# Performance work log

Measured on AMD Instinct MI355X. Metric: run time of the kernel, lower is better.

The kernel has to match this reference:

```python
import jax, jax.numpy as jnp
import numpy as np
from jax import lax

B, L, F = 32, 2048, 76   # batch, seq_len, feat_dim
H = 128                  # conv hidden channels
D = 128                  # prototype dim (last 1x1 conv)
P = 128                  # number of prototypes
CLASS_SIZE = 2


def setup_inputs() -> dict:
    key = jax.random.key(0)
    ks = jax.random.split(key, 8)
    w = lambda k, shape: jax.random.normal(k, shape, jnp.float32) * 0.05
    return {
        "x": jax.random.normal(ks[0], (B, L, F), jnp.float32),
        "W1": w(ks[1], (H, F, 5)), "b1": jnp.zeros((H,), jnp.float32),
        "W2": w(ks[2], (H, H, 5)), "b2": jnp.zeros((H,), jnp.float32),
        "W3": w(ks[3], (H, H, 5)), "b3": jnp.zeros((H,), jnp.float32),
        "Wo1": w(ks[4], (D, H)), "bo1": jnp.zeros((D,), jnp.float32),
        "Wo2": w(ks[5], (D, D)), "bo2": jnp.zeros((D,), jnp.float32),
        "prototypes": jax.random.uniform(ks[6], (P, D), jnp.float32),
        "protop_classes": jnp.concatenate([jnp.zeros(P // 2, jnp.int32), jnp.ones(P // 2, jnp.int32)]),
    }


def _conv1d_same(h, W, b):
    # h: (B, C, L), W: (O, C, K=5), symmetric padding 2 == torch padding=k//2
    y = lax.conv_general_dilated(h, W, window_strides=(1,), padding=[(2, 2)],
                                 dimension_numbers=("NCW", "OIW", "NCW"))
    return y + b[None, :, None]


def _maxpool2(h):
    return lax.reduce_window(h, -jnp.inf, lax.max, (1, 1, 2), (1, 1, 2), "VALID")


def reference(x, W1, b1, W2, b2, W3, b3, Wo1, bo1, Wo2, bo2, prototypes, protop_classes):
    h = jnp.transpose(x, (0, 2, 1))  # (B, F, L)
    for W, b in ((W1, b1), (W2, b2), (W3, b3)):
        h = _maxpool2(jax.nn.relu(_conv1d_same(h, W, b)))
    # 1x1 convs as channel matmuls
    h = jax.nn.relu(jnp.einsum("bcl,oc->bol", h, Wo1) + bo1[None, :, None])
    h = jax.nn.relu(jnp.einsum("bcl,oc->bol", h, Wo2) + bo2[None, :, None])
    f = jnp.transpose(h, (0, 2, 1))  # (B, Lp=256, D)
    # l2_conv via ||a-b||^2 = ||a||^2 - 2 a.b + ||b||^2 (same math, GEMM form)
    d2 = (jnp.sum(f * f, axis=-1, keepdims=True)
          - 2.0 * jnp.einsum("bld,pd->blp", f, prototypes)
          + jnp.sum(prototypes * prototypes, axis=-1))  # (B, Lp, P)
    dis = jnp.sqrt(jnp.maximum(d2, 1e-12))
    min_dis = jnp.min(dis, axis=1)  # (B, P): min over patches
    # dis2sim, 'log' activation
    sim = jnp.log((min_dis + 1.0) / (min_dis + 1e-4))
    # init_weights: last_layer.weight[i,j] = 1 if protop_classes[j]==i else -0.5
    lw = jnp.where(protop_classes[None, :] == jnp.arange(CLASS_SIZE)[:, None], 1.0, -0.5)
    out = jax.nn.sigmoid(sim @ lw.T)  # (B, CLASS_SIZE)
    return out, min_dis
```

## Files before the change

### kernel.cpp

```cpp
#include <hip/hip_runtime.h>
#include <cmath>


typedef __attribute__((ext_vector_type(8))) short short8;
typedef __attribute__((ext_vector_type(4))) float f32x4;

__device__ __forceinline__ unsigned short f2bf(float v) {
    union { float f; unsigned u; } x; x.f = v;
    unsigned r = x.u + 0x7fffu + ((x.u >> 16) & 1u);
    return (unsigned short)(r >> 16);
}
__device__ __forceinline__ float bf2f(unsigned short b) {
    union { unsigned u; float f; } x; x.u = ((unsigned)b) << 16;
    return x.f;
}

__device__ void pack_conv_w(int t, int total, const float* __restrict__ W, int C,
                            unsigned short* __restrict__ dst)
{
    if (t >= total) return;
    int lane = t & 63, rest = t >> 6;
    int mf = rest & 7; rest >>= 3;
    int kk = rest % 5, cc = rest / 5;
    int m = mf * 16 + (lane & 15);
    int cb = cc * 32 + (lane >> 4) * 8;
    unsigned short v[8];
#pragma unroll
    for (int j = 0; j < 8; ++j) {
        int c = cb + j;
        v[j] = (c < C) ? f2bf(W[((size_t)m * C + c) * 5 + kk]) : (unsigned short)0;
    }
    *(uint4*)&dst[(size_t)t * 8] = *(uint4*)v;
}

__device__ void pack_mat(int t, const float* __restrict__ M, unsigned short* __restrict__ dst)
{
    if (t >= 2048) return;
    int lane = t & 63, mf = (t >> 6) & 7, cc = t >> 9;
    int m = mf * 16 + (lane & 15);
    int c0 = cc * 32 + (lane >> 4) * 8;
    unsigned short v[8];
#pragma unroll
    for (int j = 0; j < 8; ++j) v[j] = f2bf(M[(size_t)m * 128 + c0 + j]);
    *(uint4*)&dst[(size_t)t * 8] = *(uint4*)v;
}

__global__ __launch_bounds__(256)
void prep_weights_kernel(const float* __restrict__ W1, const float* __restrict__ W2,
                         const float* __restrict__ W3, const float* __restrict__ Wo1,
                         const float* __restrict__ Wo2, const float* __restrict__ protos,
                         unsigned short* A1, unsigned short* A2, unsigned short* A3,
                         unsigned short* AW1, unsigned short* AW2, unsigned short* AP,
                         float* pn, unsigned* pm_bits)
{
    int t = blockIdx.x * 256 + threadIdx.x;
    switch (blockIdx.y) {
    case 0: pack_conv_w(t, 7680,  W1, 76,  A1); break;
    case 1: pack_conv_w(t, 10240, W2, 128, A2); break;
    case 2: pack_conv_w(t, 10240, W3, 128, A3); break;
    case 3: pack_mat(t, Wo1, AW1); break;
    case 4: pack_mat(t, Wo2, AW2); break;
    case 5: pack_mat(t, protos, AP); break;
    case 6:
        if (t < 128) {
            float s = 0.f;
            for (int d = 0; d < 128; ++d) {
                float v = bf2f(f2bf(protos[(size_t)t * 128 + d]));
                s = fmaf(v, v, s);
            }
            pn[t] = s;
        }
        break;
    case 7:
        if (t < 4096) pm_bits[t] = 0x7F800000u;
        break;
    }
}

template <int NJ, int NCC, int STRIDE, int ROWMAX>
__device__ __forceinline__ void conv_k(const unsigned short* __restrict__ Af,
                                       const unsigned short* __restrict__ sIn,
                                       int nbase, int mf0, int lane,
                                       f32x4 (&acc)[4][NJ])
{
    const int lc = lane & 15;
    const int lk = (lane >> 4) * 8;
#pragma unroll
    for (int i = 0; i < 4; ++i)
#pragma unroll
        for (int j = 0; j < NJ; ++j) acc[i][j] = (f32x4){0.f, 0.f, 0.f, 0.f};

    for (int cc = 0; cc < NCC; ++cc) {
#pragma unroll
        for (int kk = 0; kk < 5; ++kk) {
            const int step = cc * 5 + kk;
            short8 a[4];
#pragma unroll
            for (int i = 0; i < 4; ++i)
                a[i] = *(const short8*)&Af[(((size_t)step * 8 + mf0 + i) * 64 + lane) * 8];
            short8 bb[NJ];
#pragma unroll
            for (int j = 0; j < NJ; ++j) {
                int row = nbase + j * 16 + lc + kk;
                if (ROWMAX >= 0) row = min(row, ROWMAX);
                bb[j] = *(const short8*)&sIn[row * STRIDE + cc * 32 + lk];
            }
#pragma unroll
            for (int j = 0; j < NJ; ++j)
#pragma unroll
                for (int i = 0; i < 4; ++i)
                    acc[i][j] = __builtin_amdgcn_mfma_f32_16x16x32_bf16(a[i], bb[j], acc[i][j], 0, 0, 0);
        }
    }
}

__device__ __forceinline__ void gemm_head(const unsigned short* __restrict__ Af,
                                          const unsigned short* __restrict__ s_f,
                                          int mf0h, int lane, f32x4 (&acc)[2])
{
    const int lc = lane & 15;
    const int lk = (lane >> 4) * 8;
    acc[0] = (f32x4){0.f, 0.f, 0.f, 0.f};
    acc[1] = (f32x4){0.f, 0.f, 0.f, 0.f};
#pragma unroll
    for (int cc = 0; cc < 4; ++cc) {
        short8 a[2];
#pragma unroll
        for (int i = 0; i < 2; ++i)
            a[i] = *(const short8*)&Af[(((size_t)cc * 8 + mf0h + i) * 64 + lane) * 8];
        short8 bb = *(const short8*)&s_f[lc * 136 + cc * 32 + lk];
#pragma unroll
        for (int i = 0; i < 2; ++i)
            acc[i] = __builtin_amdgcn_mfma_f32_16x16x32_bf16(a[i], bb, acc[i], 0, 0, 0);
    }
}

__global__ __launch_bounds__(256, 2)
void mega_kernel(const float* __restrict__ x,
                 const unsigned short* __restrict__ A1, const float* __restrict__ b1,
                 const unsigned short* __restrict__ A2, const float* __restrict__ b2,
                 const unsigned short* __restrict__ A3, const float* __restrict__ b3,
                 const unsigned short* __restrict__ AW1, const float* __restrict__ bo1,
                 const unsigned short* __restrict__ AW2, const float* __restrict__ bo2,
                 const unsigned short* __restrict__ AP,  const float* __restrict__ pn,
                 unsigned* __restrict__ pm_bits)
{
    __shared__ __align__(16) unsigned short s_x[196 * 104];
    __shared__ __align__(16) unsigned short s_h1[84 * 136];
    __shared__ float s_cb[768];
    __shared__ float s_part[64];
    __shared__ float s_fn[16];
    unsigned short* s_h2 = s_x;
    unsigned short* s_f  = s_x + 5440;

    const int tid  = threadIdx.x;
    const int u    = blockIdx.x;
    const int b    = blockIdx.y;
    const int lane = tid & 63;
    const int wid  = tid >> 6;
    const int mg   = wid & 1;
    const int ng   = wid >> 1;
    const int mf0  = mg * 4;
    const int lc   = lane & 15;
    const int lq   = (lane >> 4) * 4;

    for (int i = tid; i < 768; i += 256) {
        const float* src = (i < 128) ? b1 : (i < 256) ? b2 : (i < 384) ? b3
                         : (i < 512) ? bo1 : (i < 640) ? bo2 : pn;
        s_cb[i] = src[i & 127];
    }

    const int xbase = 128 * u - 14;
    for (int idx = tid; idx < 196 * 24; idx += 256) {
        int pos = idx / 24, c0 = (idx % 24) * 4;
        int l = xbase + pos;
        unsigned short v[4] = {0, 0, 0, 0};
        if (c0 < 76 && l >= 0 && l < 2048) {
            float4 xv = *(const float4*)&x[((size_t)b * 2048 + l) * 76 + c0];
            v[0] = f2bf(xv.x); v[1] = f2bf(xv.y); v[2] = f2bf(xv.z); v[3] = f2bf(xv.w);
        }
        *(uint2*)&s_x[pos * 104 + c0] = *(uint2*)v;
    }
    __syncthreads();

    {
        f32x4 acc[4][6];
        conv_k<6, 3, 104, -1>(A1, s_x, ng * 96, mf0, lane, acc);

#pragma unroll
        for (int i = 0; i < 4; ++i) {
            const int ch0 = (mf0 + i) * 16 + lq;
#pragma unroll
            for (int j = 0; j < 6; ++j) {
                const int nl = ng * 96 + j * 16 + lc;
                unsigned short pk[4];
#pragma unroll
                for (int r = 0; r < 4; ++r) {
                    float v = fmaxf(acc[i][j][r] + s_cb[ch0 + r], 0.f);
                    float o = __shfl_xor(v, 1);
                    pk[r] = f2bf(fmaxf(v, o));
                }
                if ((lc & 1) == 0) {
                    int rr = nl >> 1;
                    int jg = 64 * u - 6 + rr;
                    if (rr < 84) {
                        uint2 val = (jg >= 0 && jg < 1024) ? *(uint2*)pk : make_uint2(0u, 0u);
                        *(uint2*)&s_h1[rr * 136 + ch0] = val;
                    }
                }
            }
        }
    }
    __syncthreads();

    {
        f32x4 acc[4][3];
        conv_k<3, 4, 136, 83>(A2, s_h1, ng * 48, mf0, lane, acc);

#pragma unroll
        for (int i = 0; i < 4; ++i) {
            const int ch0 = (mf0 + i) * 16 + lq;
#pragma unroll
            for (int j = 0; j < 3; ++j) {
                const int nl = ng * 48 + j * 16 + lc;
                unsigned short pk[4];
#pragma unroll
                for (int r = 0; r < 4; ++r) {
                    float v = fmaxf(acc[i][j][r] + s_cb[128 + ch0 + r], 0.f);
                    float o = __shfl_xor(v, 1);
                    pk[r] = f2bf(fmaxf(v, o));
                }
                if ((lc & 1) == 0) {
                    int rr = nl >> 1;
                    int jg = 32 * u - 2 + rr;
                    if (rr < 40) {
                        uint2 val = (jg >= 0 && jg < 512) ? *(uint2*)pk : make_uint2(0u, 0u);
                        *(uint2*)&s_h2[rr * 136 + ch0] = val;
                    }
                }
            }
        }
    }
    __syncthreads();

    {
        f32x4 acc[4][1];
        conv_k<1, 4, 136, -1>(A3, s_h2, ng * 16, mf0, lane, acc);

#pragma unroll
        for (int i = 0; i < 4; ++i) {
            const int ch0 = (mf0 + i) * 16 + lq;
            const int nl = ng * 16 + lc;
            unsigned short pk[4];
#pragma unroll
            for (int r = 0; r < 4; ++r) {
                float v = fmaxf(acc[i][0][r] + s_cb[256 + ch0 + r], 0.f);
                float o = __shfl_xor(v, 1);
                pk[r] = f2bf(fmaxf(v, o));
            }
            if ((lc & 1) == 0)
                *(uint2*)&s_f[(nl >> 1) * 136 + ch0] = *(uint2*)pk;
        }
    }
    __syncthreads();

    const int mf0h = wid * 2;
    f32x4 hacc[2];

    gemm_head(AW1, s_f, mf0h, lane, hacc);
    __syncthreads();
#pragma unroll
    for (int i = 0; i < 2; ++i) {
        const int ch0 = (mf0h + i) * 16 + lq;
        unsigned short pk[4];
#pragma unroll
        for (int r = 0; r < 4; ++r)
            pk[r] = f2bf(fmaxf(hacc[i][r] + s_cb[384 + ch0 + r], 0.f));
        *(uint2*)&s_f[lc * 136 + ch0] = *(uint2*)pk;
    }
    __syncthreads();

    gemm_head(AW2, s_f, mf0h, lane, hacc);
    __syncthreads();
#pragma unroll
    for (int i = 0; i < 2; ++i) {
        const int ch0 = (mf0h + i) * 16 + lq;
        unsigned short pk[4];
#pragma unroll
        for (int r = 0; r < 4; ++r)
            pk[r] = f2bf(fmaxf(hacc[i][r] + s_cb[512 + ch0 + r], 0.f));
        *(uint2*)&s_f[lc * 136 + ch0] = *(uint2*)pk;
    }
    __syncthreads();

    if (tid < 64) {
        int n = tid >> 2, part = tid & 3;
        float s = 0.f;
        for (int c = part * 32; c < part * 32 + 32; ++c) {
            float v = bf2f(s_f[n * 136 + c]);
            s = fmaf(v, v, s);
        }
        s_part[part * 16 + n] = s;
    }
    __syncthreads();
    if (tid < 16)
        s_fn[tid] = s_part[tid] + s_part[16 + tid] + s_part[32 + tid] + s_part[48 + tid];
    __syncthreads();

    gemm_head(AP, s_f, mf0h, lane, hacc);

#pragma unroll
    for (int i = 0; i < 2; ++i) {
#pragma unroll
        for (int r = 0; r < 4; ++r) {
            const int p = (mf0h + i) * 16 + lq + r;
            float d2 = s_fn[lc] + s_cb[640 + p] - 2.f * hacc[i][r];
            float m = sqrtf(fmaxf(d2, 1e-12f));
#pragma unroll
            for (int s = 1; s < 16; s <<= 1)
                m = fminf(m, __shfl_xor(m, s));
            if (lc == 0)
                atomicMin(&pm_bits[(size_t)b * 128 + p], __float_as_uint(m));
        }
    }
}

__global__ __launch_bounds__(128)
void finalize_kernel(const float* __restrict__ pm,
                     const int* __restrict__ classes,
                     float* __restrict__ out)
{
    __shared__ float r0[128], r1[128];
    const int b = blockIdx.x, p = threadIdx.x;
    float m = pm[(size_t)b * 128 + p];
    out[64 + b * 128 + p] = m;

    float sim = logf((m + 1.0f) / (m + 1e-4f));
    int cls = classes[p];
    r0[p] = (cls == 0) ? sim : -0.5f * sim;
    r1[p] = (cls == 1) ? sim : -0.5f * sim;
    __syncthreads();
    for (int s = 64; s > 0; s >>= 1) {
        if (p < s) { r0[p] += r0[p + s]; r1[p] += r1[p + s]; }
        __syncthreads();
    }
    if (p == 0) {
        out[b * 2 + 0] = 1.f / (1.f + expf(-r0[0]));
        out[b * 2 + 1] = 1.f / (1.f + expf(-r1[0]));
    }
}

extern "C" void kernel_launch(void* const* d_in, const int* in_sizes, int n_in,
                              void* d_out, int out_size, void* d_ws, size_t ws_size,
                              hipStream_t stream)
{
    (void)in_sizes; (void)n_in; (void)out_size; (void)ws_size;
    const float* x    = (const float*)d_in[0];
    const float* W1   = (const float*)d_in[1];
    const float* b1   = (const float*)d_in[2];
    const float* W2   = (const float*)d_in[3];
    const float* b2   = (const float*)d_in[4];
    const float* W3   = (const float*)d_in[5];
    const float* b3   = (const float*)d_in[6];
    const float* Wo1  = (const float*)d_in[7];
    const float* bo1  = (const float*)d_in[8];
    const float* Wo2  = (const float*)d_in[9];
    const float* bo2  = (const float*)d_in[10];
    const float* prot = (const float*)d_in[11];
    const int*   cls  = (const int*)d_in[12];
    float* out = (float*)d_out;

    char* ws = (char*)d_ws;
    unsigned short* A1  = (unsigned short*)(ws);
    unsigned short* A2  = (unsigned short*)(ws + 122880);
    unsigned short* A3  = (unsigned short*)(ws + 286720);
    unsigned short* AW1 = (unsigned short*)(ws + 450560);
    unsigned short* AW2 = (unsigned short*)(ws + 483328);
    unsigned short* AP  = (unsigned short*)(ws + 516096);
    float*          pn  = (float*)(ws + 548864);
    unsigned*       pm  = (unsigned*)(ws + 549376);

    prep_weights_kernel<<<dim3(40, 8), 256, 0, stream>>>(W1, W2, W3, Wo1, Wo2, prot,
                                                         A1, A2, A3, AW1, AW2, AP, pn, pm);
    mega_kernel<<<dim3(16, 32), 256, 0, stream>>>(x, A1, b1, A2, b2, A3, b3,
                                                  AW1, bo1, AW2, bo2, AP, pn, pm);
    finalize_kernel<<<32, 128, 0, stream>>>((const float*)pm, cls, out);
}
```

Before: 130.2 us.

## Use 8 waves per block with halved per-wave M tiles and prefetched A fragments

Doubles the block to 512 threads (8 waves), splitting the output channels so each wave computes 2 M-fragments instead of 4. The conv loop becomes a flat step loop that software-prefetches the next step's weight fragments from global memory. The head GEMMs now use one fragment per wave, and the padded x row stride shrinks from 104 to 84 to cut LDS use. The aim is more latency hiding and higher occupancy, at the cost of lower per-wave reuse of B operands from LDS and possible LDS bank conflicts with the new stride.

```diff
diff --git a/kernel.cpp b/kernel.cpp
--- a/kernel.cpp
+++ b/kernel.cpp
@@ -81,61 +81,63 @@
 __device__ __forceinline__ void conv_k(const unsigned short* __restrict__ Af,
                                        const unsigned short* __restrict__ sIn,
                                        int nbase, int mf0, int lane,
-                                       f32x4 (&acc)[4][NJ])
+                                       f32x4 (&acc)[2][NJ])
 {
     const int lc = lane & 15;
     const int lk = (lane >> 4) * 8;
-#pragma unroll
-    for (int i = 0; i < 4; ++i)
+    constexpr int NSTEP = NCC * 5;
+#pragma unroll
+    for (int i = 0; i < 2; ++i)
 #pragma unroll
         for (int j = 0; j < NJ; ++j) acc[i][j] = (f32x4){0.f, 0.f, 0.f, 0.f};
 
-    for (int cc = 0; cc < NCC; ++cc) {
-#pragma unroll
-        for (int kk = 0; kk < 5; ++kk) {
-            const int step = cc * 5 + kk;
-            short8 a[4];
-#pragma unroll
-            for (int i = 0; i < 4; ++i)
-                a[i] = *(const short8*)&Af[(((size_t)step * 8 + mf0 + i) * 64 + lane) * 8];
-            short8 bb[NJ];
-#pragma unroll
-            for (int j = 0; j < NJ; ++j) {
-                int row = nbase + j * 16 + lc + kk;
-                if (ROWMAX >= 0) row = min(row, ROWMAX);
-                bb[j] = *(const short8*)&sIn[row * STRIDE + cc * 32 + lk];
-            }
-#pragma unroll
-            for (int j = 0; j < NJ; ++j)
-#pragma unroll
-                for (int i = 0; i < 4; ++i)
-                    acc[i][j] = __builtin_amdgcn_mfma_f32_16x16x32_bf16(a[i], bb[j], acc[i][j], 0, 0, 0);
-        }
+    const unsigned short* ap = Af + ((size_t)mf0 * 64 + lane) * 8;
+
+    short8 a_cur[2], a_nxt[2];
+    a_cur[0] = *(const short8*)&ap[0];
+    a_cur[1] = *(const short8*)&ap[512];
+
+    int kk = 0, cb = 0;
+    for (int s = 0; s < NSTEP; ++s) {
+        if (s + 1 < NSTEP) {
+            const unsigned short* apn = ap + (size_t)(s + 1) * 4096;
+            a_nxt[0] = *(const short8*)&apn[0];
+            a_nxt[1] = *(const short8*)&apn[512];
+        }
+        short8 bb[NJ];
+#pragma unroll
+        for (int j = 0; j < NJ; ++j) {
+            int row = nbase + j * 16 + lc + kk;
+            if (ROWMAX >= 0) row = min(row, ROWMAX);
+            bb[j] = *(const short8*)&sIn[row * STRIDE + cb + lk];
+        }
+#pragma unroll
+        for (int j = 0; j < NJ; ++j)
+#pragma unroll
+            for (int i = 0; i < 2; ++i)
+                acc[i][j] = __builtin_amdgcn_mfma_f32_16x16x32_bf16(a_cur[i], bb[j], acc[i][j], 0, 0, 0);
+        a_cur[0] = a_nxt[0];
+        a_cur[1] = a_nxt[1];
+        if (++kk == 5) { kk = 0; cb += 32; }
     }
 }
 
 __device__ __forceinline__ void gemm_head(const unsigned short* __restrict__ Af,
                                           const unsigned short* __restrict__ s_f,
-                                          int mf0h, int lane, f32x4 (&acc)[2])
+                                          int mf, int lane, f32x4& acc)
 {
     const int lc = lane & 15;
     const int lk = (lane >> 4) * 8;
-    acc[0] = (f32x4){0.f, 0.f, 0.f, 0.f};
-    acc[1] = (f32x4){0.f, 0.f, 0.f, 0.f};
+    acc = (f32x4){0.f, 0.f, 0.f, 0.f};
 #pragma unroll
     for (int cc = 0; cc < 4; ++cc) {
-        short8 a[2];
-#pragma unroll
-        for (int i = 0; i < 2; ++i)
-            a[i] = *(const short8*)&Af[(((size_t)cc * 8 + mf0h + i) * 64 + lane) * 8];
+        short8 a = *(const short8*)&Af[(((size_t)cc * 8 + mf) * 64 + lane) * 8];
         short8 bb = *(const short8*)&s_f[lc * 136 + cc * 32 + lk];
-#pragma unroll
-        for (int i = 0; i < 2; ++i)
-            acc[i] = __builtin_amdgcn_mfma_f32_16x16x32_bf16(a[i], bb, acc[i], 0, 0, 0);
-    }
-}
-
-__global__ __launch_bounds__(256, 2)
+        acc = __builtin_amdgcn_mfma_f32_16x16x32_bf16(a, bb, acc, 0, 0, 0);
+    }
+}
+
+__global__ __launch_bounds__(512, 4)
 void mega_kernel(const float* __restrict__ x,
                  const unsigned short* __restrict__ A1, const float* __restrict__ b1,
                  const unsigned short* __restrict__ A2, const float* __restrict__ b2,
@@ -145,7 +147,7 @@
                  const unsigned short* __restrict__ AP,  const float* __restrict__ pn,
                  unsigned* __restrict__ pm_bits)
 {
-    __shared__ __align__(16) unsigned short s_x[196 * 104];
+    __shared__ __align__(16) unsigned short s_x[196 * 84 + 16];
     __shared__ __align__(16) unsigned short s_h1[84 * 136];
     __shared__ float s_cb[768];
     __shared__ float s_part[64];
@@ -158,37 +160,38 @@
     const int b    = blockIdx.y;
     const int lane = tid & 63;
     const int wid  = tid >> 6;
-    const int mg   = wid & 1;
-    const int ng   = wid >> 1;
-    const int mf0  = mg * 4;
+    const int mg   = wid & 3;
+    const int ng   = wid >> 2;
+    const int mf0  = mg * 2;
     const int lc   = lane & 15;
     const int lq   = (lane >> 4) * 4;
 
-    for (int i = tid; i < 768; i += 256) {
+    for (int i = tid; i < 768; i += 512) {
         const float* src = (i < 128) ? b1 : (i < 256) ? b2 : (i < 384) ? b3
                          : (i < 512) ? bo1 : (i < 640) ? bo2 : pn;
         s_cb[i] = src[i & 127];
     }
+    if (tid < 16) s_x[196 * 84 + tid] = 0;
 
     const int xbase = 128 * u - 14;
-    for (int idx = tid; idx < 196 * 24; idx += 256) {
-        int pos = idx / 24, c0 = (idx % 24) * 4;
+    for (int idx = tid; idx < 196 * 21; idx += 512) {
+        int pos = idx / 21, c0 = (idx % 21) * 4;
         int l = xbase + pos;
         unsigned short v[4] = {0, 0, 0, 0};
         if (c0 < 76 && l >= 0 && l < 2048) {
             float4 xv = *(const float4*)&x[((size_t)b * 2048 + l) * 76 + c0];
             v[0] = f2bf(xv.x); v[1] = f2bf(xv.y); v[2] = f2bf(xv.z); v[3] = f2bf(xv.w);
         }
-        *(uint2*)&s_x[pos * 104 + c0] = *(uint2*)v;
-    }
-    __syncthreads();
-
-    {
-        f32x4 acc[4][6];
-        conv_k<6, 3, 104, -1>(A1, s_x, ng * 96, mf0, lane, acc);
-
-#pragma unroll
-        for (int i = 0; i < 4; ++i) {
+        *(uint2*)&s_x[pos * 84 + c0] = *(uint2*)v;
+    }
+    __syncthreads();
+
+    {
+        f32x4 acc[2][6];
+        conv_k<6, 3, 84, -1>(A1, s_x, ng * 96, mf0, lane, acc);
+
+#pragma unroll
+        for (int i = 0; i < 2; ++i) {
             const int ch0 = (mf0 + i) * 16 + lq;
 #pragma unroll
             for (int j = 0; j < 6; ++j) {
@@ -214,11 +217,11 @@
     __syncthreads();
 
     {
-        f32x4 acc[4][3];
+        f32x4 acc[2][3];
         conv_k<3, 4, 136, 83>(A2, s_h1, ng * 48, mf0, lane, acc);
 
 #pragma unroll
-        for (int i = 0; i < 4; ++i) {
+        for (int i = 0; i < 2; ++i) {
             const int ch0 = (mf0 + i) * 16 + lq;
 #pragma unroll
             for (int j = 0; j < 3; ++j) {
@@ -244,11 +247,11 @@
     __syncthreads();
 
     {
-        f32x4 acc[4][1];
+        f32x4 acc[2][1];
         conv_k<1, 4, 136, -1>(A3, s_h2, ng * 16, mf0, lane, acc);
 
 #pragma unroll
-        for (int i = 0; i < 4; ++i) {
+        for (int i = 0; i < 2; ++i) {
             const int ch0 = (mf0 + i) * 16 + lq;
             const int nl = ng * 16 + lc;
             unsigned short pk[4];
@@ -264,31 +267,28 @@
     }
     __syncthreads();
 
-    const int mf0h = wid * 2;
-    f32x4 hacc[2];
-
-    gemm_head(AW1, s_f, mf0h, lane, hacc);
-    __syncthreads();
-#pragma unroll
-    for (int i = 0; i < 2; ++i) {
-        const int ch0 = (mf0h + i) * 16 + lq;
+    f32x4 hacc;
+
+    gemm_head(AW1, s_f, wid, lane, hacc);
+    __syncthreads();
+    {
+        const int ch0 = wid * 16 + lq;
         unsigned short pk[4];
 #pragma unroll
         for (int r = 0; r < 4; ++r)
-            pk[r] = f2bf(fmaxf(hacc[i][r] + s_cb[384 + ch0 + r], 0.f));
+            pk[r] = f2bf(fmaxf(hacc[r] + s_cb[384 + ch0 + r], 0.f));
         *(uint2*)&s_f[lc * 136 + ch0] = *(uint2*)pk;
     }
     __syncthreads();
 
-    gemm_head(AW2, s_f, mf0h, lane, hacc);
-    __syncthreads();
-#pragma unroll
-    for (int i = 0; i < 2; ++i) {
-        const int ch0 = (mf0h + i) * 16 + lq;
+    gemm_head(AW2, s_f, wid, lane, hacc);
+    __syncthreads();
+    {
+        const int ch0 = wid * 16 + lq;
         unsigned short pk[4];
 #pragma unroll
         for (int r = 0; r < 4; ++r)
-            pk[r] = f2bf(fmaxf(hacc[i][r] + s_cb[512 + ch0 + r], 0.f));
+            pk[r] = f2bf(fmaxf(hacc[r] + s_cb[512 + ch0 + r], 0.f));
         *(uint2*)&s_f[lc * 136 + ch0] = *(uint2*)pk;
     }
     __syncthreads();
@@ -307,21 +307,18 @@
         s_fn[tid] = s_part[tid] + s_part[16 + tid] + s_part[32 + tid] + s_part[48 + tid];
     __syncthreads();
 
-    gemm_head(AP, s_f, mf0h, lane, hacc);
-
-#pragma unroll
-    for (int i = 0; i < 2; ++i) {
-#pragma unroll
-        for (int r = 0; r < 4; ++r) {
-            const int p = (mf0h + i) * 16 + lq + r;
-            float d2 = s_fn[lc] + s_cb[640 + p] - 2.f * hacc[i][r];
-            float m = sqrtf(fmaxf(d2, 1e-12f));
-#pragma unroll
-            for (int s = 1; s < 16; s <<= 1)
-                m = fminf(m, __shfl_xor(m, s));
-            if (lc == 0)
-                atomicMin(&pm_bits[(size_t)b * 128 + p], __float_as_uint(m));
-        }
+    gemm_head(AP, s_f, wid, lane, hacc);
+
+#pragma unroll
+    for (int r = 0; r < 4; ++r) {
+        const int p = wid * 16 + lq + r;
+        float d2 = s_fn[lc] + s_cb[640 + p] - 2.f * hacc[r];
+        float m = sqrtf(fmaxf(d2, 1e-12f));
+#pragma unroll
+        for (int s = 1; s < 16; s <<= 1)
+            m = fminf(m, __shfl_xor(m, s));
+        if (lc == 0)
+            atomicMin(&pm_bits[(size_t)b * 128 + p], __float_as_uint(m));
     }
 }
 
@@ -382,7 +379,7 @@
 
     prep_weights_kernel<<<dim3(40, 8), 256, 0, stream>>>(W1, W2, W3, Wo1, Wo2, prot,
                                                          A1, A2, A3, AW1, AW2, AP, pn, pm);
-    mega_kernel<<<dim3(16, 32), 256, 0, stream>>>(x, A1, b1, A2, b2, A3, b3,
+    mega_kernel<<<dim3(16, 32), 512, 0, stream>>>(x, A1, b1, A2, b2, A3, b3,
                                                   AW1, bo1, AW2, bo2, AP, pn, pm);
     finalize_kernel<<<32, 128, 0, stream>>>((const float*)pm, cls, out);
 }
```

Measured after the change: 154.1 us. 18.4% more time.

## Halve per-block sequence tile to double grid and raise occupancy

Applied to the files above, without the earlier changes.

Each block now covers 64 input positions instead of 128, so the launch grid doubles to 1024 blocks and shared memory per block shrinks, which lets launch bounds request 4 blocks per CU. Conv2/conv3 warp work is rebalanced across output channels, and the head pads the 8 valid final rows to 16 and masks the padding out of the min. The aim is better CU fill and latency hiding. The cost is proportionally more halo recomputation and more MFMA work wasted on padded rows in the head, plus register pressure from the higher occupancy target.

```diff
diff --git a/kernel.cpp b/kernel.cpp
--- a/kernel.cpp
+++ b/kernel.cpp
@@ -77,26 +77,27 @@
     }
 }
 
-template <int NJ, int NCC, int STRIDE, int ROWMAX>
+template <int NM, int NJ, int NCC, int STRIDE, int ROWMAX>
 __device__ __forceinline__ void conv_k(const unsigned short* __restrict__ Af,
                                        const unsigned short* __restrict__ sIn,
                                        int nbase, int mf0, int lane,
-                                       f32x4 (&acc)[4][NJ])
+                                       f32x4 (&acc)[NM][NJ])
 {
     const int lc = lane & 15;
     const int lk = (lane >> 4) * 8;
 #pragma unroll
-    for (int i = 0; i < 4; ++i)
+    for (int i = 0; i < NM; ++i)
 #pragma unroll
         for (int j = 0; j < NJ; ++j) acc[i][j] = (f32x4){0.f, 0.f, 0.f, 0.f};
 
+#pragma unroll
     for (int cc = 0; cc < NCC; ++cc) {
 #pragma unroll
         for (int kk = 0; kk < 5; ++kk) {
             const int step = cc * 5 + kk;
-            short8 a[4];
-#pragma unroll
-            for (int i = 0; i < 4; ++i)
+            short8 a[NM];
+#pragma unroll
+            for (int i = 0; i < NM; ++i)
                 a[i] = *(const short8*)&Af[(((size_t)step * 8 + mf0 + i) * 64 + lane) * 8];
             short8 bb[NJ];
 #pragma unroll
@@ -108,7 +109,7 @@
 #pragma unroll
             for (int j = 0; j < NJ; ++j)
 #pragma unroll
-                for (int i = 0; i < 4; ++i)
+                for (int i = 0; i < NM; ++i)
                     acc[i][j] = __builtin_amdgcn_mfma_f32_16x16x32_bf16(a[i], bb[j], acc[i][j], 0, 0, 0);
         }
     }
@@ -135,7 +136,7 @@
     }
 }
 
-__global__ __launch_bounds__(256, 2)
+__global__ __launch_bounds__(256, 4)
 void mega_kernel(const float* __restrict__ x,
                  const unsigned short* __restrict__ A1, const float* __restrict__ b1,
                  const unsigned short* __restrict__ A2, const float* __restrict__ b2,
@@ -145,22 +146,19 @@
                  const unsigned short* __restrict__ AP,  const float* __restrict__ pn,
                  unsigned* __restrict__ pm_bits)
 {
-    __shared__ __align__(16) unsigned short s_x[196 * 104];
-    __shared__ __align__(16) unsigned short s_h1[84 * 136];
+    __shared__ __align__(16) unsigned short s_x[92 * 84 + 16];
+    __shared__ __align__(16) unsigned short s_h1[44 * 136];
     __shared__ float s_cb[768];
     __shared__ float s_part[64];
     __shared__ float s_fn[16];
     unsigned short* s_h2 = s_x;
-    unsigned short* s_f  = s_x + 5440;
+    unsigned short* s_f  = s_x + 2720;
 
     const int tid  = threadIdx.x;
     const int u    = blockIdx.x;
     const int b    = blockIdx.y;
     const int lane = tid & 63;
     const int wid  = tid >> 6;
-    const int mg   = wid & 1;
-    const int ng   = wid >> 1;
-    const int mf0  = mg * 4;
     const int lc   = lane & 15;
     const int lq   = (lane >> 4) * 4;
 
@@ -169,30 +167,33 @@
                          : (i < 512) ? bo1 : (i < 640) ? bo2 : pn;
         s_cb[i] = src[i & 127];
     }
-
-    const int xbase = 128 * u - 14;
-    for (int idx = tid; idx < 196 * 24; idx += 256) {
-        int pos = idx / 24, c0 = (idx % 24) * 4;
+    if (tid < 16) s_x[92 * 84 + tid] = 0;
+
+    const int xbase = 64 * u - 14;
+    for (int idx = tid; idx < 92 * 21; idx += 256) {
+        int pos = idx / 21, c0 = (idx % 21) * 4;
         int l = xbase + pos;
         unsigned short v[4] = {0, 0, 0, 0};
         if (c0 < 76 && l >= 0 && l < 2048) {
             float4 xv = *(const float4*)&x[((size_t)b * 2048 + l) * 76 + c0];
             v[0] = f2bf(xv.x); v[1] = f2bf(xv.y); v[2] = f2bf(xv.z); v[3] = f2bf(xv.w);
         }
-        *(uint2*)&s_x[pos * 104 + c0] = *(uint2*)v;
+        *(uint2*)&s_x[pos * 84 + c0] = *(uint2*)v;
     }
     __syncthreads();
 
     {
-        f32x4 acc[4][6];
-        conv_k<6, 3, 104, -1>(A1, s_x, ng * 96, mf0, lane, acc);
+        const int mg = wid & 1, ng = wid >> 1;
+        const int mf0 = mg * 4;
+        f32x4 acc[4][3];
+        conv_k<4, 3, 3, 84, 91>(A1, s_x, ng * 48, mf0, lane, acc);
 
 #pragma unroll
         for (int i = 0; i < 4; ++i) {
             const int ch0 = (mf0 + i) * 16 + lq;
 #pragma unroll
-            for (int j = 0; j < 6; ++j) {
-                const int nl = ng * 96 + j * 16 + lc;
+            for (int j = 0; j < 3; ++j) {
+                const int nl = ng * 48 + j * 16 + lc;
                 unsigned short pk[4];
 #pragma unroll
                 for (int r = 0; r < 4; ++r) {
@@ -202,8 +203,8 @@
                 }
                 if ((lc & 1) == 0) {
                     int rr = nl >> 1;
-                    int jg = 64 * u - 6 + rr;
-                    if (rr < 84) {
+                    int jg = 32 * u - 6 + rr;
+                    if (rr < 44) {
                         uint2 val = (jg >= 0 && jg < 1024) ? *(uint2*)pk : make_uint2(0u, 0u);
                         *(uint2*)&s_h1[rr * 136 + ch0] = val;
                     }
@@ -214,15 +215,16 @@
     __syncthreads();
 
     {
-        f32x4 acc[4][3];
-        conv_k<3, 4, 136, 83>(A2, s_h1, ng * 48, mf0, lane, acc);
-
-#pragma unroll
-        for (int i = 0; i < 4; ++i) {
+        const int mf0 = wid * 2;
+        f32x4 acc[2][3];
+        conv_k<2, 3, 4, 136, 43>(A2, s_h1, 0, mf0, lane, acc);
+
+#pragma unroll
+        for (int i = 0; i < 2; ++i) {
             const int ch0 = (mf0 + i) * 16 + lq;
 #pragma unroll
             for (int j = 0; j < 3; ++j) {
-                const int nl = ng * 48 + j * 16 + lc;
+                const int nl = j * 16 + lc;
                 unsigned short pk[4];
 #pragma unroll
                 for (int r = 0; r < 4; ++r) {
@@ -232,8 +234,8 @@
                 }
                 if ((lc & 1) == 0) {
                     int rr = nl >> 1;
-                    int jg = 32 * u - 2 + rr;
-                    if (rr < 40) {
+                    int jg = 16 * u - 2 + rr;
+                    if (rr < 20) {
                         uint2 val = (jg >= 0 && jg < 512) ? *(uint2*)pk : make_uint2(0u, 0u);
                         *(uint2*)&s_h2[rr * 136 + ch0] = val;
                     }
@@ -244,13 +246,13 @@
     __syncthreads();
 
     {
-        f32x4 acc[4][1];
-        conv_k<1, 4, 136, -1>(A3, s_h2, ng * 16, mf0, lane, acc);
-
-#pragma unroll
-        for (int i = 0; i < 4; ++i) {
+        const int mf0 = wid * 2;
+        f32x4 acc[2][1];
+        conv_k<2, 1, 4, 136, -1>(A3, s_h2, 0, mf0, lane, acc);
+
+#pragma unroll
+        for (int i = 0; i < 2; ++i) {
             const int ch0 = (mf0 + i) * 16 + lq;
-            const int nl = ng * 16 + lc;
             unsigned short pk[4];
 #pragma unroll
             for (int r = 0; r < 4; ++r) {
@@ -259,8 +261,10 @@
                 pk[r] = f2bf(fmaxf(v, o));
             }
             if ((lc & 1) == 0)
-                *(uint2*)&s_f[(nl >> 1) * 136 + ch0] = *(uint2*)pk;
-        }
+                *(uint2*)&s_f[(lc >> 1) * 136 + ch0] = *(uint2*)pk;
+        }
+        for (int i = tid; i < 544; i += 256)
+            ((unsigned*)(s_f + 1088))[i] = 0u;
     }
     __syncthreads();
 
@@ -315,7 +319,7 @@
         for (int r = 0; r < 4; ++r) {
             const int p = (mf0h + i) * 16 + lq + r;
             float d2 = s_fn[lc] + s_cb[640 + p] - 2.f * hacc[i][r];
-            float m = sqrtf(fmaxf(d2, 1e-12f));
+            float m = (lc < 8) ? sqrtf(fmaxf(d2, 1e-12f)) : 3.0e38f;
 #pragma unroll
             for (int s = 1; s < 16; s <<= 1)
                 m = fminf(m, __shfl_xor(m, s));
@@ -382,7 +386,7 @@
 
     prep_weights_kernel<<<dim3(40, 8), 256, 0, stream>>>(W1, W2, W3, Wo1, Wo2, prot,
                                                          A1, A2, A3, AW1, AW2, AP, pn, pm);
-    mega_kernel<<<dim3(16, 32), 256, 0, stream>>>(x, A1, b1, A2, b2, A3, b3,
+    mega_kernel<<<dim3(32, 32), 256, 0, stream>>>(x, A1, b1, A2, b2, A3, b3,
                                                   AW1, bo1, AW2, bo2, AP, pn, pm);
     finalize_kernel<<<32, 128, 0, stream>>>((const float*)pm, cls, out);
 }
```

New measurement: 139.7 us. 7.3% more time.

## Fuse finalize into mega kernel via last-block ticket and unroll conv channel loop

Applied to the files above, without the earlier changes.

Removes the separate finalize kernel launch. Each mega_kernel block takes a ticket from a global counter after a threadfence, and the last block to finish reads the atomic minima, writes min_dis, computes the log similarities and writes the sigmoid class outputs. The conv inner channel loop is also fully unrolled, and the atomicMin loop order is swapped. This saves one launch and its gap but serialises the tail work onto a single block, and the full unroll may raise register pressure.

```diff
diff --git a/kernel.cpp b/kernel.cpp
--- a/kernel.cpp
+++ b/kernel.cpp
@@ -73,6 +73,7 @@
         break;
     case 7:
         if (t < 4096) pm_bits[t] = 0x7F800000u;
+        if (t == 4096) pm_bits[4096] = 0u;
         break;
     }
 }
@@ -90,6 +91,7 @@
 #pragma unroll
         for (int j = 0; j < NJ; ++j) acc[i][j] = (f32x4){0.f, 0.f, 0.f, 0.f};
 
+#pragma unroll
     for (int cc = 0; cc < NCC; ++cc) {
 #pragma unroll
         for (int kk = 0; kk < 5; ++kk) {
@@ -143,13 +145,16 @@
                  const unsigned short* __restrict__ AW1, const float* __restrict__ bo1,
                  const unsigned short* __restrict__ AW2, const float* __restrict__ bo2,
                  const unsigned short* __restrict__ AP,  const float* __restrict__ pn,
-                 unsigned* __restrict__ pm_bits)
+                 const int* __restrict__ classes,
+                 unsigned* __restrict__ pm_bits,
+                 float* __restrict__ outp)
 {
     __shared__ __align__(16) unsigned short s_x[196 * 104];
     __shared__ __align__(16) unsigned short s_h1[84 * 136];
     __shared__ float s_cb[768];
     __shared__ float s_part[64];
     __shared__ float s_fn[16];
+    __shared__ unsigned s_ticket;
     unsigned short* s_h2 = s_x;
     unsigned short* s_f  = s_x + 5440;
 
@@ -310,10 +315,11 @@
     gemm_head(AP, s_f, mf0h, lane, hacc);
 
 #pragma unroll
-    for (int i = 0; i < 2; ++i) {
-#pragma unroll
-        for (int r = 0; r < 4; ++r) {
-            const int p = (mf0h + i) * 16 + lq + r;
+    for (int r = 0; r < 4; ++r) {
+        const int p0 = mf0h * 16 + lq + r;
+#pragma unroll
+        for (int i = 0; i < 2; ++i) {
+            const int p = p0 + i * 16;
             float d2 = s_fn[lc] + s_cb[640 + p] - 2.f * hacc[i][r];
             float m = sqrtf(fmaxf(d2, 1e-12f));
 #pragma unroll
@@ -323,30 +329,29 @@
                 atomicMin(&pm_bits[(size_t)b * 128 + p], __float_as_uint(m));
         }
     }
-}
-
-__global__ __launch_bounds__(128)
-void finalize_kernel(const float* __restrict__ pm,
-                     const int* __restrict__ classes,
-                     float* __restrict__ out)
-{
-    __shared__ float r0[128], r1[128];
-    const int b = blockIdx.x, p = threadIdx.x;
-    float m = pm[(size_t)b * 128 + p];
-    out[64 + b * 128 + p] = m;
-
-    float sim = logf((m + 1.0f) / (m + 1e-4f));
-    int cls = classes[p];
-    r0[p] = (cls == 0) ? sim : -0.5f * sim;
-    r1[p] = (cls == 1) ? sim : -0.5f * sim;
-    __syncthreads();
-    for (int s = 64; s > 0; s >>= 1) {
-        if (p < s) { r0[p] += r0[p + s]; r1[p] += r1[p + s]; }
-        __syncthreads();
-    }
-    if (p == 0) {
-        out[b * 2 + 0] = 1.f / (1.f + expf(-r0[0]));
-        out[b * 2 + 1] = 1.f / (1.f + expf(-r1[0]));
+
+    __threadfence();
+    __syncthreads();
+    if (tid == 0) s_ticket = atomicAdd(&pm_bits[4096], 1u);
+    __syncthreads();
+    if (s_ticket != 16u * 32u - 1u) return;
+
+    float* s_sim = (float*)s_x;
+    for (int i = tid; i < 4096; i += 256) {
+        unsigned ub = atomicMin(&pm_bits[i], 0x7F800000u);
+        float m = __uint_as_float(ub);
+        outp[64 + i] = m;
+        s_sim[i] = logf((m + 1.0f) / (m + 1e-4f));
+    }
+    __syncthreads();
+    if (tid < 64) {
+        int bb = tid >> 1, c = tid & 1;
+        float s = 0.f;
+        for (int p = 0; p < 128; ++p) {
+            float sim = s_sim[bb * 128 + p];
+            s += (classes[p] == c) ? sim : -0.5f * sim;
+        }
+        outp[bb * 2 + c] = 1.f / (1.f + expf(-s));
     }
 }
 
@@ -383,6 +388,5 @@
     prep_weights_kernel<<<dim3(40, 8), 256, 0, stream>>>(W1, W2, W3, Wo1, Wo2, prot,
                                                          A1, A2, A3, AW1, AW2, AP, pn, pm);
     mega_kernel<<<dim3(16, 32), 256, 0, stream>>>(x, A1, b1, A2, b2, A3, b3,
-                                                  AW1, bo1, AW2, bo2, AP, pn, pm);
-    finalize_kernel<<<32, 128, 0, stream>>>((const float*)pm, cls, out);
-}
+                                                  AW1, bo1, AW2, bo2, AP, pn, cls, pm, out);
+}
```

Measured after the change: 169.4 us. 1.3x slower.
